# Performance work log

Hardware: AMD Instinct MI355X
Metric: run time of the kernel (lower is better)

Reference implementation:

```python
import jax, jax.numpy as jnp
import numpy as np

B, NPG, C, DEG, DE = 64, 1024, 512, 32, 16  # graphs, nodes/graph, feat dim, avg degree, edge-feat dim
N = B * NPG
E = N * DEG
RATIO = 0.5


def setup_inputs() -> dict:
    key = jax.random.key(0)
    k1, k2, k3, k4 = jax.random.split(key, 4)
    x = jax.random.normal(k1, (N, C), dtype=jnp.float32)
    # edges drawn within each graph block so batch structure is respected
    local = jax.random.randint(k2, (2, E), 0, NPG, dtype=jnp.int32)
    offsets = jnp.repeat(jnp.arange(B, dtype=jnp.int32) * NPG, NPG * DEG)
    edge_index = local + offsets[None, :]
    edge_attr = jax.random.normal(k3, (E, DE), dtype=jnp.float32)
    batch = jnp.repeat(jnp.arange(B, dtype=jnp.int32), NPG)
    W = jax.random.normal(k4, (C, 1), dtype=jnp.float32) * (1.0 / np.sqrt(C))
    b = jnp.zeros((1,), dtype=jnp.float32)
    return {"x": x, "edge_index": edge_index, "edge_attr": edge_attr, "batch": batch,
            "W": W, "b": b, "num_graphs": B, "nodes_per_graph": NPG}


def _gcn_score(x, edge_index, W, b):
    # PyG GCNConv(in_channels, 1): add self-loops, symmetric D^-1/2 (A+I) D^-1/2 norm
    n = x.shape[0]
    loop = jnp.arange(n, dtype=edge_index.dtype)
    s = jnp.concatenate([edge_index[0], loop])
    d = jnp.concatenate([edge_index[1], loop])
    deg = jnp.zeros((n,), x.dtype).at[d].add(jnp.ones((), x.dtype))  # >= 1 via self loops
    dinv = jax.lax.rsqrt(deg)
    norm = dinv[s] * dinv[d]                       # [E+n]
    h = (x @ W)[:, 0]                               # project first: [n]
    score = jnp.zeros((n,), x.dtype).at[d].add(h[s] * norm) + b[0]
    return score


def reference(x, edge_index, edge_attr, batch, W, b, num_graphs, nodes_per_graph):
    n = x.shape[0]
    k = int(np.ceil(RATIO * nodes_per_graph))
    score = _gcn_score(x, edge_index, W, b)         # [n]
    # per-graph top-k (equal-sized graphs -> fixed-shape top_k over [B, NPG])
    sc = score.reshape(num_graphs, nodes_per_graph)
    _, topi = jax.lax.top_k(sc, k)                  # [B, k], score-descending per graph
    offs = (jnp.arange(num_graphs, dtype=edge_index.dtype) * nodes_per_graph)[:, None]
    perm = (topi.astype(edge_index.dtype) + offs).reshape(-1)  # [B*k]
    x_new = x[perm] * jnp.tanh(score[perm])[:, None]
    batch_new = batch[perm]
    # filter_adj: keep edges with both endpoints selected, remap to new ids.
    # Fixed-shape version: full-length edge list with invalid entries = -1 plus a mask.
    sel = jnp.zeros((n,), bool).at[perm].set(True)
    newidx = jnp.full((n,), -1, edge_index.dtype).at[perm].set(
        jnp.arange(perm.shape[0], dtype=edge_index.dtype))
    src, dst = edge_index[0], edge_index[1]
    edge_mask = sel[src] & sel[dst]                 # [E]
    ei_new = jnp.where(edge_mask[None, :], jnp.stack([newidx[src], newidx[dst]]), -1)
    ea_new = jnp.where(edge_mask[:, None], edge_attr, jnp.zeros((), edge_attr.dtype))
    return x_new, ei_new, ea_new, edge_mask, batch_new, perm
```

## Files before the change

### kernel.cpp

```cpp
#include <hip/hip_runtime.h>
#include <math.h>

#define N_NODES 65536
#define C_DIM   512
#define E_EDGES 2097152
#define DE_DIM  16
#define B_GR    64
#define NPG     1024
#define DEG     32
#define EPG     (NPG * DEG)
#define PARTS   4
#define EPP     (EPG / PARTS)
#define K_SEL   512
#define NK      (B_GR * K_SEL)

#define OUT_XNEW  0
#define OUT_EI    (NK * C_DIM)
#define OUT_EA    (OUT_EI + 2 * E_EDGES)
#define OUT_MASK  (OUT_EA + (size_t)E_EDGES * DE_DIM)
#define OUT_BATCH (OUT_MASK + E_EDGES)
#define OUT_PERM  (OUT_BATCH + NK)

__global__ void k_proj(const float* __restrict__ x,
                       const float* __restrict__ W,
                       float* __restrict__ h,
                       float* __restrict__ score,
                       float* __restrict__ deg,
                       int*   __restrict__ newidx) {
    __shared__ float sW[C_DIM];
    const int t = threadIdx.x;
    ((float2*)sW)[t] = ((const float2*)W)[t];
    __syncthreads();

    const int wave = t >> 6, lane = t & 63;
    const int node = blockIdx.x * 4 + wave;
    const float* xr = x + (size_t)node * C_DIM + lane * 8;
    float4 a0 = ((const float4*)xr)[0];
    float4 a1 = ((const float4*)xr)[1];
    const float* wr = sW + lane * 8;
    float s = a0.x * wr[0] + a0.y * wr[1] + a0.z * wr[2] + a0.w * wr[3]
            + a1.x * wr[4] + a1.y * wr[5] + a1.z * wr[6] + a1.w * wr[7];
#pragma unroll
    for (int off = 32; off > 0; off >>= 1) s += __shfl_down(s, off, 64);
    if (lane == 0) h[node] = s;

    const int gid = blockIdx.x * 256 + t;
    if (gid < N_NODES) {
        score[gid]  = 0.0f;
        deg[gid]    = 1.0f;
        newidx[gid] = -1;
    }
}

__global__ void __launch_bounds__(1024)
k_deg_part(const int* __restrict__ dst, float* __restrict__ deg) {
    __shared__ float dgp[NPG];
    const int bg = blockIdx.x;
    const int g = bg >> 2, part = bg & 3;
    const int t = threadIdx.x;
    dgp[t] = 0.0f;
    __syncthreads();

    const int4* d4 = (const int4*)(dst + g * EPG + part * EPP);
    int4 a = d4[t], b = d4[1024 + t];
    atomicAdd(&dgp[a.x & (NPG - 1)], 1.0f);
    atomicAdd(&dgp[a.y & (NPG - 1)], 1.0f);
    atomicAdd(&dgp[a.z & (NPG - 1)], 1.0f);
    atomicAdd(&dgp[a.w & (NPG - 1)], 1.0f);
    atomicAdd(&dgp[b.x & (NPG - 1)], 1.0f);
    atomicAdd(&dgp[b.y & (NPG - 1)], 1.0f);
    atomicAdd(&dgp[b.z & (NPG - 1)], 1.0f);
    atomicAdd(&dgp[b.w & (NPG - 1)], 1.0f);
    __syncthreads();

    atomicAdd(&deg[g * NPG + t], dgp[t]);
}

__global__ void __launch_bounds__(1024)
k_score_part(const int* __restrict__ src, const int* __restrict__ dst,
             const float* __restrict__ h, const float* __restrict__ deg,
             float* __restrict__ score) {
    __shared__ float hs[NPG];
    __shared__ float di[NPG];
    __shared__ float scp[NPG];
    const int bg = blockIdx.x;
    const int g = bg >> 2, part = bg & 3;
    const int t = threadIdx.x;
    const int nbase = g * NPG;

    hs[t]  = h[nbase + t];
    di[t]  = rsqrtf(deg[nbase + t]);
    scp[t] = 0.0f;
    __syncthreads();

    const int4* s4 = (const int4*)(src + g * EPG + part * EPP);
    const int4* d4 = (const int4*)(dst + g * EPG + part * EPP);
    int4 sa = s4[t], sb = s4[1024 + t];
    int4 da = d4[t], db = d4[1024 + t];
    {
        int s0 = sa.x & (NPG-1), d0 = da.x & (NPG-1);
        int s1 = sa.y & (NPG-1), d1 = da.y & (NPG-1);
        int s2 = sa.z & (NPG-1), d2 = da.z & (NPG-1);
        int s3 = sa.w & (NPG-1), d3 = da.w & (NPG-1);
        atomicAdd(&scp[d0], hs[s0] * di[s0] * di[d0]);
        atomicAdd(&scp[d1], hs[s1] * di[s1] * di[d1]);
        atomicAdd(&scp[d2], hs[s2] * di[s2] * di[d2]);
        atomicAdd(&scp[d3], hs[s3] * di[s3] * di[d3]);
    }
    {
        int s0 = sb.x & (NPG-1), d0 = db.x & (NPG-1);
        int s1 = sb.y & (NPG-1), d1 = db.y & (NPG-1);
        int s2 = sb.z & (NPG-1), d2 = db.z & (NPG-1);
        int s3 = sb.w & (NPG-1), d3 = db.w & (NPG-1);
        atomicAdd(&scp[d0], hs[s0] * di[s0] * di[d0]);
        atomicAdd(&scp[d1], hs[s1] * di[s1] * di[d1]);
        atomicAdd(&scp[d2], hs[s2] * di[s2] * di[d2]);
        atomicAdd(&scp[d3], hs[s3] * di[s3] * di[d3]);
    }
    __syncthreads();

    atomicAdd(&score[nbase + t], scp[t]);
}

__global__ void __launch_bounds__(1024)
k_topk(const float* __restrict__ score, const float* __restrict__ h,
       const float* __restrict__ deg, const float* __restrict__ b,
       int*   __restrict__ newidx, int* __restrict__ permw,
       float* __restrict__ mult,
       float* __restrict__ out_perm, float* __restrict__ out_batch) {
    __shared__ float scs[NPG];
    __shared__ unsigned long long keys[NPG];
    const int g = blockIdx.x, t = threadIdx.x;
    const int nbase = g * NPG;

    {
        const float dv  = rsqrtf(deg[nbase + t]);
        const float scf = score[nbase + t] + h[nbase + t] * dv * dv + b[0];
        scs[t] = scf;
        const unsigned int bits = __float_as_uint(scf);
        const unsigned int u = bits ^ ((bits & 0x80000000u) ? 0xFFFFFFFFu : 0x80000000u);
        keys[t] = ((unsigned long long)(~u) << 32) | (unsigned int)t;
    }
    __syncthreads();

    for (int k = 2; k <= NPG; k <<= 1) {
        for (int j = k >> 1; j > 0; j >>= 1) {
            if (t < NPG / 2) {
                const int i = ((t & ~(j - 1)) << 1) | (t & (j - 1));
                const int p = i | j;
                const bool asc = (i & k) == 0;
                const unsigned long long a = keys[i], bb = keys[p];
                if ((a > bb) == asc) { keys[i] = bb; keys[p] = a; }
            }
            __syncthreads();
        }
    }

    if (t < K_SEL) {
        const int li   = (int)(keys[t] & 0xFFFFFFFFull);
        const int node = nbase + li;
        const int j    = g * K_SEL + t;
        permw[j]     = node;
        newidx[node] = j;
        mult[j]      = tanhf(scs[li]);
        out_perm[j]  = (float)node;
        out_batch[j] = (float)g;
    }
}

#define EDGE_BLKS (E_EDGES / 64)
#define XNEW_BLKS (NK / 2)

__global__ void k_tail(const float* __restrict__ x,
                       const float* __restrict__ mult,
                       const int* __restrict__ permw,
                       const int* __restrict__ src,
                       const int* __restrict__ dst,
                       const float* __restrict__ ea,
                       const int* __restrict__ newidx,
                       float* __restrict__ out_xnew,
                       float* __restrict__ out_ei,
                       float* __restrict__ out_ea,
                       float* __restrict__ out_mask) {
    int bid = blockIdx.x;
    if (bid < EDGE_BLKS) {
        const int gid = bid * 256 + threadIdx.x;
        const int e = gid >> 2, c = gid & 3;
        const int s = src[e], d = dst[e];
        const int ns = newidx[s], nd = newidx[d];
        const bool m = (ns >= 0) && (nd >= 0);

        float4 v = make_float4(0.f, 0.f, 0.f, 0.f);
        if (m) v = ((const float4*)ea)[(size_t)e * 4 + c];
        ((float4*)out_ea)[(size_t)e * 4 + c] = v;

        if (c == 0) {
            out_ei[e]           = m ? (float)ns : -1.0f;
            out_ei[E_EDGES + e] = m ? (float)nd : -1.0f;
            out_mask[e]         = m ? 1.0f : 0.0f;
        }
    } else {
        bid -= EDGE_BLKS;
        const int row = bid * 2 + (threadIdx.x >> 7);
        const int c   = (threadIdx.x & 127) * 4;
        const int node = permw[row];
        const float tt = mult[row];
        float4 v = *(const float4*)(x + (size_t)node * C_DIM + c);
        v.x *= tt; v.y *= tt; v.z *= tt; v.w *= tt;
        *(float4*)(out_xnew + (size_t)row * C_DIM + c) = v;
    }
}

extern "C" void kernel_launch(void* const* d_in, const int* in_sizes, int n_in,
                              void* d_out, int out_size, void* d_ws, size_t ws_size,
                              hipStream_t stream) {
    const float* x  = (const float*)d_in[0];
    const int*   ei = (const int*)d_in[1];
    const float* ea = (const float*)d_in[2];
    const float* W  = (const float*)d_in[4];
    const float* b  = (const float*)d_in[5];
    const int* src = ei;
    const int* dst = ei + E_EDGES;

    float* out = (float*)d_out;

    float* h      = (float*)d_ws;
    float* score  = h + N_NODES;
    float* deg    = score + N_NODES;
    int*   newidx = (int*)(deg + N_NODES);
    int*   permw  = newidx + N_NODES;
    float* mult   = (float*)(permw + NK);

    k_proj<<<N_NODES / 4, 256, 0, stream>>>(x, W, h, score, deg, newidx);
    k_deg_part<<<B_GR * PARTS, 1024, 0, stream>>>(dst, deg);
    k_score_part<<<B_GR * PARTS, 1024, 0, stream>>>(src, dst, h, deg, score);
    k_topk<<<B_GR, 1024, 0, stream>>>(score, h, deg, b, newidx, permw, mult,
                                      out + OUT_PERM, out + OUT_BATCH);
    k_tail<<<EDGE_BLKS + XNEW_BLKS, 256, 0, stream>>>(x, mult, permw, src, dst, ea,
                                                      newidx, out + OUT_XNEW,
                                                      out + OUT_EI, out + OUT_EA,
                                                      out + OUT_MASK);
}
```

Baseline: 462.3 us.

## Fuse degree histogram into projection kernel and merge scoring with top-k

The degree histogram now runs as 64 extra blocks inside the projection kernel and writes inverse sqrt degrees directly. The scatter-add score computation moves into the per-graph top-k kernel, so one block per graph accumulates all of its edges in shared memory with unsafe float atomics. Folding the norm into h*dinv removes the global score/deg init and the global atomics. The score phase now runs on only 64 blocks instead of 256, which may reduce parallelism for the edge scatter. newidx for unselected nodes is set to -1 in the select kernel.

New measurement: 481.6 us. 4.2% more time.

```diff
diff --git a/kernel.cpp b/kernel.cpp
--- a/kernel.cpp
+++ b/kernel.cpp
@@ -9,8 +9,6 @@
 #define NPG     1024
 #define DEG     32
 #define EPG     (NPG * DEG)
-#define PARTS   4
-#define EPP     (EPG / PARTS)
 #define K_SEL   512
 #define NK      (B_GR * K_SEL)
 
@@ -21,121 +19,92 @@
 #define OUT_BATCH (OUT_MASK + E_EDGES)
 #define OUT_PERM  (OUT_BATCH + NK)
 
-__global__ void k_proj(const float* __restrict__ x,
-                       const float* __restrict__ W,
-                       float* __restrict__ h,
-                       float* __restrict__ score,
-                       float* __restrict__ deg,
-                       int*   __restrict__ newidx) {
+#define HIST_BLKS B_GR
+
+__global__ void k_front(const float* __restrict__ x,
+                        const float* __restrict__ W,
+                        const int* __restrict__ dst,
+                        float* __restrict__ h,
+                        float* __restrict__ di) {
+    __shared__ int   cnt[NPG];
     __shared__ float sW[C_DIM];
-    const int t = threadIdx.x;
-    ((float2*)sW)[t] = ((const float2*)W)[t];
-    __syncthreads();
-
-    const int wave = t >> 6, lane = t & 63;
-    const int node = blockIdx.x * 4 + wave;
-    const float* xr = x + (size_t)node * C_DIM + lane * 8;
-    float4 a0 = ((const float4*)xr)[0];
-    float4 a1 = ((const float4*)xr)[1];
-    const float* wr = sW + lane * 8;
-    float s = a0.x * wr[0] + a0.y * wr[1] + a0.z * wr[2] + a0.w * wr[3]
-            + a1.x * wr[4] + a1.y * wr[5] + a1.z * wr[6] + a1.w * wr[7];
-#pragma unroll
-    for (int off = 32; off > 0; off >>= 1) s += __shfl_down(s, off, 64);
-    if (lane == 0) h[node] = s;
-
-    const int gid = blockIdx.x * 256 + t;
-    if (gid < N_NODES) {
-        score[gid]  = 0.0f;
-        deg[gid]    = 1.0f;
-        newidx[gid] = -1;
+
+    if (blockIdx.x < HIST_BLKS) {
+        const int g = blockIdx.x, t = threadIdx.x;
+#pragma unroll
+        for (int i = 0; i < 4; ++i) cnt[t + 256 * i] = 0;
+        __syncthreads();
+
+        const int4* dv = (const int4*)(dst + (size_t)g * EPG);
+#pragma unroll
+        for (int i = 0; i < 32; ++i) {
+            int4 a = dv[t + 256 * i];
+            atomicAdd(&cnt[a.x & (NPG - 1)], 1);
+            atomicAdd(&cnt[a.y & (NPG - 1)], 1);
+            atomicAdd(&cnt[a.z & (NPG - 1)], 1);
+            atomicAdd(&cnt[a.w & (NPG - 1)], 1);
+        }
+        __syncthreads();
+
+#pragma unroll
+        for (int i = 0; i < 4; ++i) {
+            const int n = t + 256 * i;
+            di[(size_t)g * NPG + n] = rsqrtf((float)cnt[n] + 1.0f);
+        }
+    } else {
+        const int t = threadIdx.x;
+        ((float2*)sW)[t] = ((const float2*)W)[t];
+        __syncthreads();
+
+        const int wave = t >> 6, lane = t & 63;
+        const int node = (blockIdx.x - HIST_BLKS) * 4 + wave;
+        const float* xr = x + (size_t)node * C_DIM + lane * 8;
+        float4 a0 = ((const float4*)xr)[0];
+        float4 a1 = ((const float4*)xr)[1];
+        const float* wr = sW + lane * 8;
+        float s = a0.x * wr[0] + a0.y * wr[1] + a0.z * wr[2] + a0.w * wr[3]
+                + a1.x * wr[4] + a1.y * wr[5] + a1.z * wr[6] + a1.w * wr[7];
+#pragma unroll
+        for (int off = 32; off > 0; off >>= 1) s += __shfl_down(s, off, 64);
+        if (lane == 0) h[node] = s;
     }
 }
 
 __global__ void __launch_bounds__(1024)
-k_deg_part(const int* __restrict__ dst, float* __restrict__ deg) {
-    __shared__ float dgp[NPG];
-    const int bg = blockIdx.x;
-    const int g = bg >> 2, part = bg & 3;
-    const int t = threadIdx.x;
-    dgp[t] = 0.0f;
-    __syncthreads();
-
-    const int4* d4 = (const int4*)(dst + g * EPG + part * EPP);
-    int4 a = d4[t], b = d4[1024 + t];
-    atomicAdd(&dgp[a.x & (NPG - 1)], 1.0f);
-    atomicAdd(&dgp[a.y & (NPG - 1)], 1.0f);
-    atomicAdd(&dgp[a.z & (NPG - 1)], 1.0f);
-    atomicAdd(&dgp[a.w & (NPG - 1)], 1.0f);
-    atomicAdd(&dgp[b.x & (NPG - 1)], 1.0f);
-    atomicAdd(&dgp[b.y & (NPG - 1)], 1.0f);
-    atomicAdd(&dgp[b.z & (NPG - 1)], 1.0f);
-    atomicAdd(&dgp[b.w & (NPG - 1)], 1.0f);
-    __syncthreads();
-
-    atomicAdd(&deg[g * NPG + t], dgp[t]);
-}
-
-__global__ void __launch_bounds__(1024)
-k_score_part(const int* __restrict__ src, const int* __restrict__ dst,
-             const float* __restrict__ h, const float* __restrict__ deg,
-             float* __restrict__ score) {
-    __shared__ float hs[NPG];
-    __shared__ float di[NPG];
+k_select(const int* __restrict__ src, const int* __restrict__ dst,
+         const float* __restrict__ h, const float* __restrict__ di,
+         const float* __restrict__ b,
+         int*   __restrict__ newidx, int* __restrict__ permw,
+         float* __restrict__ mult,
+         float* __restrict__ out_perm, float* __restrict__ out_batch) {
+    __shared__ float hd[NPG];
     __shared__ float scp[NPG];
-    const int bg = blockIdx.x;
-    const int g = bg >> 2, part = bg & 3;
-    const int t = threadIdx.x;
+    __shared__ float scs[NPG];
+    __shared__ unsigned long long keys[NPG];
+
+    const int g = blockIdx.x, t = threadIdx.x;
     const int nbase = g * NPG;
 
-    hs[t]  = h[nbase + t];
-    di[t]  = rsqrtf(deg[nbase + t]);
+    const float di_t = di[nbase + t];
+    hd[t]  = h[nbase + t] * di_t;
     scp[t] = 0.0f;
     __syncthreads();
 
-    const int4* s4 = (const int4*)(src + g * EPG + part * EPP);
-    const int4* d4 = (const int4*)(dst + g * EPG + part * EPP);
-    int4 sa = s4[t], sb = s4[1024 + t];
-    int4 da = d4[t], db = d4[1024 + t];
+    const int4* sv = (const int4*)(src + (size_t)g * EPG);
+    const int4* dv = (const int4*)(dst + (size_t)g * EPG);
+#pragma unroll
+    for (int i = 0; i < 8; ++i) {
+        int4 sa = sv[t + NPG * i];
+        int4 da = dv[t + NPG * i];
+        unsafeAtomicAdd(&scp[da.x & (NPG - 1)], hd[sa.x & (NPG - 1)]);
+        unsafeAtomicAdd(&scp[da.y & (NPG - 1)], hd[sa.y & (NPG - 1)]);
+        unsafeAtomicAdd(&scp[da.z & (NPG - 1)], hd[sa.z & (NPG - 1)]);
+        unsafeAtomicAdd(&scp[da.w & (NPG - 1)], hd[sa.w & (NPG - 1)]);
+    }
+    __syncthreads();
+
     {
-        int s0 = sa.x & (NPG-1), d0 = da.x & (NPG-1);
-        int s1 = sa.y & (NPG-1), d1 = da.y & (NPG-1);
-        int s2 = sa.z & (NPG-1), d2 = da.z & (NPG-1);
-        int s3 = sa.w & (NPG-1), d3 = da.w & (NPG-1);
-        atomicAdd(&scp[d0], hs[s0] * di[s0] * di[d0]);
-        atomicAdd(&scp[d1], hs[s1] * di[s1] * di[d1]);
-        atomicAdd(&scp[d2], hs[s2] * di[s2] * di[d2]);
-        atomicAdd(&scp[d3], hs[s3] * di[s3] * di[d3]);
-    }
-    {
-        int s0 = sb.x & (NPG-1), d0 = db.x & (NPG-1);
-        int s1 = sb.y & (NPG-1), d1 = db.y & (NPG-1);
-        int s2 = sb.z & (NPG-1), d2 = db.z & (NPG-1);
-        int s3 = sb.w & (NPG-1), d3 = db.w & (NPG-1);
-        atomicAdd(&scp[d0], hs[s0] * di[s0] * di[d0]);
-        atomicAdd(&scp[d1], hs[s1] * di[s1] * di[d1]);
-        atomicAdd(&scp[d2], hs[s2] * di[s2] * di[d2]);
-        atomicAdd(&scp[d3], hs[s3] * di[s3] * di[d3]);
-    }
-    __syncthreads();
-
-    atomicAdd(&score[nbase + t], scp[t]);
-}
-
-__global__ void __launch_bounds__(1024)
-k_topk(const float* __restrict__ score, const float* __restrict__ h,
-       const float* __restrict__ deg, const float* __restrict__ b,
-       int*   __restrict__ newidx, int* __restrict__ permw,
-       float* __restrict__ mult,
-       float* __restrict__ out_perm, float* __restrict__ out_batch) {
-    __shared__ float scs[NPG];
-    __shared__ unsigned long long keys[NPG];
-    const int g = blockIdx.x, t = threadIdx.x;
-    const int nbase = g * NPG;
-
-    {
-        const float dv  = rsqrtf(deg[nbase + t]);
-        const float scf = score[nbase + t] + h[nbase + t] * dv * dv + b[0];
+        const float scf = (scp[t] + hd[t]) * di_t + b[0];
         scs[t] = scf;
         const unsigned int bits = __float_as_uint(scf);
         const unsigned int u = bits ^ ((bits & 0x80000000u) ? 0xFFFFFFFFu : 0x80000000u);
@@ -156,15 +125,17 @@
         }
     }
 
+    const int li   = (int)(keys[t] & 0xFFFFFFFFull);
+    const int node = nbase + li;
     if (t < K_SEL) {
-        const int li   = (int)(keys[t] & 0xFFFFFFFFull);
-        const int node = nbase + li;
-        const int j    = g * K_SEL + t;
+        const int j  = g * K_SEL + t;
         permw[j]     = node;
         newidx[node] = j;
         mult[j]      = tanhf(scs[li]);
         out_perm[j]  = (float)node;
         out_batch[j] = (float)g;
+    } else {
+        newidx[node] = -1;
     }
 }
 
@@ -225,17 +196,15 @@
     float* out = (float*)d_out;
 
     float* h      = (float*)d_ws;
-    float* score  = h + N_NODES;
-    float* deg    = score + N_NODES;
-    int*   newidx = (int*)(deg + N_NODES);
-    int*   permw  = newidx + N_NODES;
-    float* mult   = (float*)(permw + NK);
-
-    k_proj<<<N_NODES / 4, 256, 0, stream>>>(x, W, h, score, deg, newidx);
-    k_deg_part<<<B_GR * PARTS, 1024, 0, stream>>>(dst, deg);
-    k_score_part<<<B_GR * PARTS, 1024, 0, stream>>>(src, dst, h, deg, score);
-    k_topk<<<B_GR, 1024, 0, stream>>>(score, h, deg, b, newidx, permw, mult,
-                                      out + OUT_PERM, out + OUT_BATCH);
+    float* di     = h + N_NODES;
+    float* mult   = di + N_NODES;
+    int*   permw  = (int*)(mult + NK);
+    int*   newidx = permw + NK;
+
+    k_front<<<HIST_BLKS + N_NODES / 4, 256, 0, stream>>>(x, W, dst, h, di);
+    k_select<<<B_GR, 1024, 0, stream>>>(src, dst, h, di, b,
+                                        newidx, permw, mult,
+                                        out + OUT_PERM, out + OUT_BATCH);
     k_tail<<<EDGE_BLKS + XNEW_BLKS, 256, 0, stream>>>(x, mult, permw, src, dst, ea,
                                                       newidx, out + OUT_XNEW,
                                                       out + OUT_EI, out + OUT_EA,
```
